# Kernel optimization log

Hardware: AMD Instinct MI355X
Metric: run time of the kernel (lower is better)

Reference implementation:

```python
import jax, jax.numpy as jnp
import numpy as np

B, T, C = 4, 2048, 1024
H = 16
D = C // H  # 64


def setup_inputs() -> dict:
    key = jax.random.key(0)
    k1, k2, k3 = jax.random.split(key, 3)
    x = jax.random.normal(k1, (B, T, C), dtype=jnp.float32)
    w_qkv = jax.random.normal(k2, (C, 3 * C), dtype=jnp.float32) * (C ** -0.5)
    b_qkv = jnp.zeros((3 * C,), dtype=jnp.float32)
    w_proj = jax.random.normal(k3, (C, C), dtype=jnp.float32) * (C ** -0.5)
    b_proj = jnp.zeros((C,), dtype=jnp.float32)
    return {"x": x, "w_qkv": w_qkv, "b_qkv": b_qkv, "w_proj": w_proj, "b_proj": b_proj}


def reference(x, w_qkv, b_qkv, w_proj, b_proj):
    qkv = x @ w_qkv + b_qkv                      # [B,T,3C]
    q, k, v = jnp.split(qkv, 3, axis=-1)
    # [B,T,C] -> [B,H,T,D]
    q = q.reshape(B, T, H, D).transpose(0, 2, 1, 3)
    k = k.reshape(B, T, H, D).transpose(0, 2, 1, 3)
    v = v.reshape(B, T, H, D).transpose(0, 2, 1, 3)
    scale = 1.0 / jnp.sqrt(jnp.float32(D))
    att = jnp.einsum('bhqd,bhkd->bhqk', q, k) * scale  # [B,H,T,T]
    causal = jnp.tril(jnp.ones((T, T), dtype=bool))
    att = jnp.where(causal[None, None], att, -jnp.inf)
    att = jax.nn.softmax(att, axis=-1)
    y = jnp.einsum('bhqk,bhkd->bhqd', att, v)          # [B,H,T,D]
    y = y.transpose(0, 2, 1, 3).reshape(B, T, C)
    return y @ w_proj + b_proj
```

## Files before the change

### kernel.cpp

```cpp
#include <hip/hip_runtime.h>
#include <hip/hip_bf16.h>
#include <stdint.h>

#define B_ 4
#define T_ 2048
#define C_ 1024
#define H_ 16
#define D_ 64

typedef __bf16 bf16;
typedef _Float16 f16;
typedef __attribute__((ext_vector_type(8))) __bf16 bf16x8;
typedef __attribute__((ext_vector_type(4))) __bf16 bf16x4;
typedef __attribute__((ext_vector_type(4))) _Float16 f16x4;
typedef __attribute__((ext_vector_type(8))) _Float16 f16x8;
typedef __attribute__((ext_vector_type(4))) float floatx4;

__device__ __forceinline__ floatx4 mfma16(bf16x8 a, bf16x8 b, floatx4 c) {
  return __builtin_amdgcn_mfma_f32_16x16x32_bf16(a, b, c, 0, 0, 0);
}
__device__ __forceinline__ floatx4 mfma_pv32(f16x8 a, f16x8 b, floatx4 c) {
  return __builtin_amdgcn_mfma_f32_16x16x32_f16(a, b, c, 0, 0, 0);
}

__device__ __forceinline__ void gl_lds16(const void* g, void* l) {
  __builtin_amdgcn_global_load_lds(
      (__attribute__((address_space(1))) uint32_t*)g,
      (__attribute__((address_space(3))) uint32_t*)l, 16, 0, 0);
}

__device__ __forceinline__ void tr_tile(const float* __restrict__ in,
                                        bf16* __restrict__ out, int K, int N,
                                        int n0, int k0, bf16 (*tile)[33]) {
  const int r = threadIdx.x >> 5, c = threadIdx.x & 31;
#pragma unroll
  for (int i = 0; i < 4; i++)
    tile[r + i * 8][c] = (bf16)in[(size_t)(k0 + r + i * 8) * N + n0 + c];
  __syncthreads();
#pragma unroll
  for (int i = 0; i < 4; i++)
    out[(size_t)(n0 + r + i * 8) * K + k0 + c] = tile[c][r + i * 8];
}

__global__ __launch_bounds__(256) void preproc(const float* __restrict__ x,
                                               bf16* __restrict__ xb,
                                               const float* __restrict__ w_qkv,
                                               bf16* __restrict__ wqkv_t,
                                               const float* __restrict__ w_proj,
                                               bf16* __restrict__ wproj_t) {
  __shared__ bf16 tile[32][33];
  const int bid = blockIdx.x;
  if (bid < 8192) {
    const size_t i = ((size_t)bid * 256 + threadIdx.x) * 4;
    const floatx4 v = *(const floatx4*)(x + i);
    bf16x4 r;
#pragma unroll
    for (int j = 0; j < 4; j++) r[j] = (bf16)v[j];
    *(bf16x4*)(xb + i) = r;
  } else if (bid < 11264) {
    const int rem = bid - 8192;
    tr_tile(w_qkv, wqkv_t, 1024, 3072, (rem % 96) * 32, (rem / 96) * 32, tile);
  } else {
    const int rem = bid - 11264;
    tr_tile(w_proj, wproj_t, 1024, 1024, (rem % 32) * 32, (rem / 32) * 32, tile);
  }
}

template <int MODE>
__global__ __launch_bounds__(256) void gemm128(const bf16* __restrict__ A,
                                               const bf16* __restrict__ Bt,
                                               const float* __restrict__ bias,
                                               void* __restrict__ o0,
                                               bf16* __restrict__ o1,
                                               f16* __restrict__ o2,
                                               int M, int N, int K) {
  __shared__ __align__(16) bf16 As[2][128 * 32];
  __shared__ __align__(16) bf16 Bs[2][128 * 32];
  const int tid = threadIdx.x;

  int bx, by;
  if (MODE == 0) {
    const int id = blockIdx.x + blockIdx.y * 64;
    const int xcd = id & 7, r = id >> 3;
    bx = xcd * 8 + (r & 7);
    by = r >> 3;
  } else {
    const int id = blockIdx.x + blockIdx.y * 8;
    const int xcd = id & 7, r = id >> 3;
    bx = r & 7;
    by = xcd * 8 + (r >> 3);
  }
  const int m0 = by * 128, n0 = bx * 128;

  const int lane = tid & 63, wv = tid >> 6;
  const int wm = (wv >> 1) * 64, wn = (wv & 1) * 64;
  const int col = lane & 15, quad = lane >> 4;

  floatx4 acc[4][4];
#pragma unroll
  for (int i = 0; i < 4; i++)
#pragma unroll
    for (int j = 0; j < 4; j++) acc[i][j] = (floatx4){0.f, 0.f, 0.f, 0.f};

  const int c0 = tid, c1 = tid + 256;
  const bf16* a0 = A + (size_t)(m0 + (c0 >> 2)) * K + (c0 & 3) * 8;
  const bf16* a1 = A + (size_t)(m0 + (c1 >> 2)) * K + (c1 & 3) * 8;
  const bf16* b0 = Bt + (size_t)(n0 + (c0 >> 2)) * K + (c0 & 3) * 8;
  const bf16* b1 = Bt + (size_t)(n0 + (c1 >> 2)) * K + (c1 & 3) * 8;

  for (int kt = 0; kt < K; kt += 64) {
#pragma unroll
    for (int hf = 0; hf < 2; hf++) {
      const int ko = kt + hf * 32;
      gl_lds16(a0 + ko, &As[hf][(wv * 64) * 8]);
      gl_lds16(a1 + ko, &As[hf][(wv * 64 + 256) * 8]);
      gl_lds16(b0 + ko, &Bs[hf][(wv * 64) * 8]);
      gl_lds16(b1 + ko, &Bs[hf][(wv * 64 + 256) * 8]);
    }
    __syncthreads();
#pragma unroll
    for (int hf = 0; hf < 2; hf++) {
      bf16x8 afr[4], bg[4];
#pragma unroll
      for (int mb = 0; mb < 4; mb++)
        afr[mb] = *(const bf16x8*)&As[hf][(wm + mb * 16 + col) * 32 + quad * 8];
#pragma unroll
      for (int nb = 0; nb < 4; nb++)
        bg[nb] = *(const bf16x8*)&Bs[hf][(wn + nb * 16 + col) * 32 + quad * 8];
#pragma unroll
      for (int mb = 0; mb < 4; mb++)
#pragma unroll
        for (int nb = 0; nb < 4; nb++)
          acc[mb][nb] = mfma16(afr[mb], bg[nb], acc[mb][nb]);
    }
    __syncthreads();
  }

#pragma unroll
  for (int mb = 0; mb < 4; mb++) {
    const int mgq = m0 + wm + mb * 16 + quad * 4;
    if (MODE == 0) {
      const int third = mgq >> 10;
      const int nn0 = mgq & 1023;
      const int h = nn0 >> 6, d0 = nn0 & 63;
      float bs[4];
#pragma unroll
      for (int r = 0; r < 4; r++) bs[r] = bias[mgq + r];
#pragma unroll
      for (int nb = 0; nb < 4; nb++) {
        const int t = n0 + wn + nb * 16 + col;
        const int bb = t >> 11, tt = t & 2047;
        const size_t bh = (size_t)bb * H_ + h;
        float v[4];
#pragma unroll
        for (int r = 0; r < 4; r++) v[r] = acc[mb][nb][r] + bs[r];
        if (third == 0) {
          bf16x4 y;
#pragma unroll
          for (int r = 0; r < 4; r++) y[r] = (bf16)v[r];
          *(bf16x4*)&((bf16*)o0)[(bh * T_ + tt) * D_ + d0] = y;
        } else if (third == 1) {
          const int lane2 = (tt & 15) | (((d0 >> 3) & 3) << 4);
          const size_t idx =
              ((((bh * 64 + (tt >> 5)) * 2 + ((tt >> 4) & 1)) * 2 + (d0 >> 5)) * 64 +
               lane2) * 8 + (d0 & 7);
          bf16x4 y;
#pragma unroll
          for (int r = 0; r < 4; r++) y[r] = (bf16)v[r];
          *(bf16x4*)&o1[idx] = y;
        } else {
#pragma unroll
          for (int r = 0; r < 4; r++) {
            const int d = d0 + r;
            const int lane2 = (d & 15) | (((tt >> 2) & 3) << 4);
            const size_t idx =
                (((bh * 64 + (tt >> 5)) * 4 + (d >> 4)) * 64 + lane2) * 8 +
                ((tt >> 4) & 1) * 4 + (tt & 3);
            o2[idx] = (f16)v[r];
          }
        }
      }
    } else {
#pragma unroll
      for (int nb = 0; nb < 4; nb++) {
        const int ng = n0 + wn + nb * 16 + col;
        const float bsc = bias[ng];
#pragma unroll
        for (int r = 0; r < 4; r++)
          ((float*)o0)[(size_t)(mgq + r) * N + ng] = acc[mb][nb][r] + bsc;
      }
    }
  }
}

__global__ __launch_bounds__(256, 2) void attn(const bf16* __restrict__ Q,
                                               const bf16* __restrict__ Kp,
                                               const f16* __restrict__ Vp,
                                               bf16* __restrict__ Y) {
  const int tid = threadIdx.x, lane = tid & 63, wv = tid >> 6;
  const int col = lane & 15, quad = lane >> 4;
  const int id = blockIdx.x;
  const int j = id >> 3;
  const int bh = ((j & 7) << 3) | (id & 7);
  const int qb = 31 - (j >> 3);
  const int b = bh >> 4, h = bh & 15;
  const int qbase = qb * 64;

  __shared__ __align__(16) floatx4 mbuf[3][16][64];
  __shared__ float lbuf[3][4][64];

  bf16x8 qf[4][2];
#pragma unroll
  for (int mq = 0; mq < 4; mq++) {
    const bf16* qp = Q + ((size_t)bh * T_ + qbase + mq * 16 + col) * D_ + quad * 8;
    qf[mq][0] = *(const bf16x8*)qp;
    qf[mq][1] = *(const bf16x8*)(qp + 32);
  }

  floatx4 o[4][4];
  float lsum[4] = {0.f, 0.f, 0.f, 0.f};
#pragma unroll
  for (int mq = 0; mq < 4; mq++)
#pragma unroll
    for (int s = 0; s < 4; s++) o[mq][s] = (floatx4){0.f, 0.f, 0.f, 0.f};

  const float C1 = 0.18033688f;
  const float C2 = 11.541560f;

  const int ktmax = qb * 2 + 1;
  const int nmine = (ktmax >= wv) ? ((ktmax - wv) >> 2) + 1 : 0;

  for (int i = 0; i < nmine; i++) {
    const int kt = wv + 4 * i;
    const bf16* kbase = Kp + ((size_t)bh * 64 + kt) * 2048 + lane * 8;
    const f16* vbase = Vp + ((size_t)bh * 64 + kt) * 2048 + lane * 8;
    bf16x8 ka[2][2];
    ka[0][0] = *(const bf16x8*)(kbase);
    ka[0][1] = *(const bf16x8*)(kbase + 512);
    ka[1][0] = *(const bf16x8*)(kbase + 1024);
    ka[1][1] = *(const bf16x8*)(kbase + 1536);
    f16x8 vv[4];
#pragma unroll
    for (int sub = 0; sub < 4; sub++) vv[sub] = *(const f16x8*)(vbase + sub * 512);

    __builtin_amdgcn_s_setprio(1);
    f16x8 pf8[4];
#pragma unroll
    for (int mq = 0; mq < 4; mq++) pf8[mq] = (f16x8){};

#pragma unroll
    for (int st = 0; st < 2; st++) {
      const int kk = kt * 2 + st;
#pragma unroll
      for (int mq = 0; mq < 4; mq++) {
        const int qq = qb * 4 + mq;
        if (kk > qq) continue;
        floatx4 s = (floatx4){0.f, 0.f, 0.f, 0.f};
        s = mfma16(ka[st][0], qf[mq][0], s);
        s = mfma16(ka[st][1], qf[mq][1], s);
        float ps = 0.f;
        const bool diag = (kk == qq);
#pragma unroll
        for (int r = 0; r < 4; r++) {
          float p = exp2f(fmaf(s[r], C1, -C2));
          if (diag && (quad * 4 + r > col)) p = 0.f;
          ps += p;
          pf8[mq][st * 4 + r] = (f16)p;
        }
        lsum[mq] += ps;
      }
    }
#pragma unroll
    for (int mq = 0; mq < 4; mq++) {
      if (kt * 2 > qb * 4 + mq) continue;
#pragma unroll
      for (int sub = 0; sub < 4; sub++)
        o[mq][sub] = mfma_pv32(vv[sub], pf8[mq], o[mq][sub]);
    }
    __builtin_amdgcn_s_setprio(0);
  }

  if (wv != 0) {
#pragma unroll
    for (int mq = 0; mq < 4; mq++) {
#pragma unroll
      for (int sub = 0; sub < 4; sub++) mbuf[wv - 1][mq * 4 + sub][lane] = o[mq][sub];
      lbuf[wv - 1][mq][lane] = lsum[mq];
    }
  }
  __syncthreads();
  if (wv == 0) {
#pragma unroll
    for (int w = 0; w < 3; w++)
#pragma unroll
      for (int mq = 0; mq < 4; mq++) {
#pragma unroll
        for (int sub = 0; sub < 4; sub++) o[mq][sub] += mbuf[w][mq * 4 + sub][lane];
        lsum[mq] += lbuf[w][mq][lane];
      }
#pragma unroll
    for (int mq = 0; mq < 4; mq++) {
      lsum[mq] += __shfl_xor(lsum[mq], 16);
      lsum[mq] += __shfl_xor(lsum[mq], 32);
      const float rinv = 1.f / lsum[mq];
      const int qrow = qbase + mq * 16 + col;
#pragma unroll
      for (int sub = 0; sub < 4; sub++) {
        bf16x4 yv;
#pragma unroll
        for (int r = 0; r < 4; r++) yv[r] = (bf16)(o[mq][sub][r] * rinv);
        *(bf16x4*)&Y[((size_t)b * T_ + qrow) * C_ + h * 64 + sub * 16 + quad * 4] = yv;
      }
    }
  }
}

extern "C" void kernel_launch(void* const* d_in, const int* in_sizes, int n_in,
                              void* d_out, int out_size, void* d_ws, size_t ws_size,
                              hipStream_t stream) {
  (void)in_sizes; (void)n_in; (void)out_size; (void)ws_size;
  const float* x      = (const float*)d_in[0];
  const float* w_qkv  = (const float*)d_in[1];
  const float* b_qkv  = (const float*)d_in[2];
  const float* w_proj = (const float*)d_in[3];
  const float* b_proj = (const float*)d_in[4];

  char* ws = (char*)d_ws;
  bf16* wqkv_t  = (bf16*)(ws);
  bf16* wproj_t = (bf16*)(ws + 6291456);
  bf16* qb      = (bf16*)(ws + 8388608);
  bf16* kbuf    = (bf16*)(ws + 25165824);
  f16*  vtbuf   = (f16*)(ws + 41943040);
  bf16* yb      = (bf16*)(ws + 58720256);
  bf16* xb      = (bf16*)(ws + 58720256);

  preproc<<<12288, 256, 0, stream>>>(x, xb, w_qkv, wqkv_t, w_proj, wproj_t);
  gemm128<0><<<dim3(64, 24), 256, 0, stream>>>(wqkv_t, xb, b_qkv, qb, kbuf, vtbuf,
                                               3072, 8192, 1024);
  attn<<<dim3(2048), 256, 0, stream>>>(qb, kbuf, vtbuf, yb);
  gemm128<1><<<dim3(8, 64), 256, 0, stream>>>(yb, wproj_t, b_proj, d_out, nullptr,
                                              nullptr, 8192, 1024, 1024);
}
```

Baseline: 262.6 us.

## Use one wave per attention block with register double-buffered K/V loads

The attention kernel drops from four waves per block to a single wave, which walks every key tile itself. This removes the shared-memory cross-wave reduction and the block barrier. K/V tiles are prefetched one iteration ahead into alternating register buffers to overlap loads with MFMA work. In exchange, each block's serial work grows about fourfold, fewer waves run per CU, and double buffering raises register pressure.

Result: slower. 276.0 us (+5.1%).

```diff
diff --git a/kernel.cpp b/kernel.cpp
--- a/kernel.cpp
+++ b/kernel.cpp
@@ -193,11 +193,11 @@
   }
 }
 
-__global__ __launch_bounds__(256, 2) void attn(const bf16* __restrict__ Q,
-                                               const bf16* __restrict__ Kp,
-                                               const f16* __restrict__ Vp,
-                                               bf16* __restrict__ Y) {
-  const int tid = threadIdx.x, lane = tid & 63, wv = tid >> 6;
+__global__ __launch_bounds__(64, 2) void attn(const bf16* __restrict__ Q,
+                                              const bf16* __restrict__ Kp,
+                                              const f16* __restrict__ Vp,
+                                              bf16* __restrict__ Y) {
+  const int lane = threadIdx.x;
   const int col = lane & 15, quad = lane >> 4;
   const int id = blockIdx.x;
   const int j = id >> 3;
@@ -206,9 +206,6 @@
   const int b = bh >> 4, h = bh & 15;
   const int qbase = qb * 64;
 
-  __shared__ __align__(16) floatx4 mbuf[3][16][64];
-  __shared__ float lbuf[3][4][64];
-
   bf16x8 qf[4][2];
 #pragma unroll
   for (int mq = 0; mq < 4; mq++) {
@@ -227,27 +224,25 @@
   const float C1 = 0.18033688f;
   const float C2 = 11.541560f;
 
-  const int ktmax = qb * 2 + 1;
-  const int nmine = (ktmax >= wv) ? ((ktmax - wv) >> 2) + 1 : 0;
-
-  for (int i = 0; i < nmine; i++) {
-    const int kt = wv + 4 * i;
-    const bf16* kbase = Kp + ((size_t)bh * 64 + kt) * 2048 + lane * 8;
-    const f16* vbase = Vp + ((size_t)bh * 64 + kt) * 2048 + lane * 8;
-    bf16x8 ka[2][2];
+  const bf16* kroot = Kp + (size_t)bh * 64 * 2048 + lane * 8;
+  const f16* vroot = Vp + (size_t)bh * 64 * 2048 + lane * 8;
+
+  auto loadkv = [&](int kt, bf16x8(&ka)[2][2], f16x8(&vv)[4]) {
+    const bf16* kbase = kroot + (size_t)kt * 2048;
+    const f16* vbase = vroot + (size_t)kt * 2048;
     ka[0][0] = *(const bf16x8*)(kbase);
     ka[0][1] = *(const bf16x8*)(kbase + 512);
     ka[1][0] = *(const bf16x8*)(kbase + 1024);
     ka[1][1] = *(const bf16x8*)(kbase + 1536);
-    f16x8 vv[4];
 #pragma unroll
     for (int sub = 0; sub < 4; sub++) vv[sub] = *(const f16x8*)(vbase + sub * 512);
-
+  };
+
+  auto compute = [&](int kt, bf16x8(&ka)[2][2], f16x8(&vv)[4]) {
     __builtin_amdgcn_s_setprio(1);
     f16x8 pf8[4];
 #pragma unroll
     for (int mq = 0; mq < 4; mq++) pf8[mq] = (f16x8){};
-
 #pragma unroll
     for (int st = 0; st < 2; st++) {
       const int kk = kt * 2 + st;
@@ -278,39 +273,36 @@
         o[mq][sub] = mfma_pv32(vv[sub], pf8[mq], o[mq][sub]);
     }
     __builtin_amdgcn_s_setprio(0);
-  }
-
-  if (wv != 0) {
-#pragma unroll
-    for (int mq = 0; mq < 4; mq++) {
-#pragma unroll
-      for (int sub = 0; sub < 4; sub++) mbuf[wv - 1][mq * 4 + sub][lane] = o[mq][sub];
-      lbuf[wv - 1][mq][lane] = lsum[mq];
-    }
-  }
-  __syncthreads();
-  if (wv == 0) {
-#pragma unroll
-    for (int w = 0; w < 3; w++)
-#pragma unroll
-      for (int mq = 0; mq < 4; mq++) {
-#pragma unroll
-        for (int sub = 0; sub < 4; sub++) o[mq][sub] += mbuf[w][mq * 4 + sub][lane];
-        lsum[mq] += lbuf[w][mq][lane];
-      }
-#pragma unroll
-    for (int mq = 0; mq < 4; mq++) {
-      lsum[mq] += __shfl_xor(lsum[mq], 16);
-      lsum[mq] += __shfl_xor(lsum[mq], 32);
-      const float rinv = 1.f / lsum[mq];
-      const int qrow = qbase + mq * 16 + col;
-#pragma unroll
-      for (int sub = 0; sub < 4; sub++) {
-        bf16x4 yv;
-#pragma unroll
-        for (int r = 0; r < 4; r++) yv[r] = (bf16)(o[mq][sub][r] * rinv);
-        *(bf16x4*)&Y[((size_t)b * T_ + qrow) * C_ + h * 64 + sub * 16 + quad * 4] = yv;
-      }
+  };
+
+  const int ktmax = qb * 2 + 1;
+  bf16x8 kaA[2][2], kaB[2][2];
+  f16x8 vvA[4], vvB[4];
+  loadkv(0, kaA, vvA);
+  int kt = 0;
+  while (true) {
+    if (kt + 1 <= ktmax) loadkv(kt + 1, kaB, vvB);
+    compute(kt, kaA, vvA);
+    kt++;
+    if (kt > ktmax) break;
+    if (kt + 1 <= ktmax) loadkv(kt + 1, kaA, vvA);
+    compute(kt, kaB, vvB);
+    kt++;
+    if (kt > ktmax) break;
+  }
+
+#pragma unroll
+  for (int mq = 0; mq < 4; mq++) {
+    lsum[mq] += __shfl_xor(lsum[mq], 16);
+    lsum[mq] += __shfl_xor(lsum[mq], 32);
+    const float rinv = 1.f / lsum[mq];
+    const int qrow = qbase + mq * 16 + col;
+#pragma unroll
+    for (int sub = 0; sub < 4; sub++) {
+      bf16x4 yv;
+#pragma unroll
+      for (int r = 0; r < 4; r++) yv[r] = (bf16)(o[mq][sub][r] * rinv);
+      *(bf16x4*)&Y[((size_t)b * T_ + qrow) * C_ + h * 64 + sub * 16 + quad * 4] = yv;
     }
   }
 }
@@ -337,7 +329,7 @@
   preproc<<<12288, 256, 0, stream>>>(x, xb, w_qkv, wqkv_t, w_proj, wproj_t);
   gemm128<0><<<dim3(64, 24), 256, 0, stream>>>(wqkv_t, xb, b_qkv, qb, kbuf, vtbuf,
                                                3072, 8192, 1024);
-  attn<<<dim3(2048), 256, 0, stream>>>(qb, kbuf, vtbuf, yb);
+  attn<<<dim3(2048), 64, 0, stream>>>(qb, kbuf, vtbuf, yb);
   gemm128<1><<<dim3(8, 64), 256, 0, stream>>>(yb, wproj_t, b_proj, d_out, nullptr,
                                               nullptr, 8192, 1024, 1024);
 }
```
